# Performance work log

Hardware: AMD Instinct MI355X
Metric: run time of the kernel (lower is better)

Reference implementation:

```python
import jax, jax.numpy as jnp
import numpy as np


def _laplacian(A):
    # D^{-1/2} A D^{-1/2}; original builds diag matrices and does D@A@D,
    # which is mathematically identical to broadcast row/col scaling.
    d = jnp.sum(A, axis=-1)
    dinv = 1.0 / jnp.sqrt(d)
    return A * dinv[:, None] * dinv[None, :]


def _poly(A, theta):
    # P = I + sum_{i=1..k} theta_sig[i-1] * A^i  (theta passed through sigmoid)
    t = jax.nn.sigmoid(theta)
    N = A.shape[-1]
    P = jnp.eye(N, dtype=A.dtype)
    seg = P
    for i in range(theta.shape[0]):  # k is small (2), static loop over poly order
        seg = seg @ A
        P = P + seg * t[i]
    return P


def setup_inputs() -> dict:
    key = jax.random.key(0)
    k1, k2, k3, k4 = jax.random.split(key, 4)
    N, DIN, DOUT, K_CHEB = 4096, 64, 64, 2
    return {
        "x": jax.random.normal(k1, (N, DIN), dtype=jnp.float32),
        "A": jax.random.uniform(k2, (N, N), dtype=jnp.float32),  # positive row sums
        "theta": jax.random.normal(k3, (K_CHEB,), dtype=jnp.float32),
        "W": jax.random.normal(k4, (DOUT, DIN), dtype=jnp.float32) / np.float32(np.sqrt(DIN)),
        "b": jnp.zeros((DOUT,), dtype=jnp.float32),
        "k": 4,
    }


def reference(x, A, theta, W, b, k):
    S = _laplacian(A)
    S = _poly(S, theta)
    S = _laplacian(S)
    # double argsort over last dim = per-row descending rank of each entry
    rank = jnp.argsort(jnp.argsort(-S, axis=-1), axis=-1)
    mask = jnp.where(rank < k, jnp.float32(1.0), jnp.float32(0.0))
    S = S * mask  # keep only top-k entries per row
    x = S @ x     # [N,N] @ [N,DIN]
    return x @ W.T + b  # nn.Linear
```

## Files before the change

### kernel.cpp

```cpp
#include <hip/hip_runtime.h>
#include <hip/hip_bf16.h>
#include <float.h>
#include <math.h>

#define N 4096
#define DIN 64

typedef signed char i8_t;
typedef signed char i8x4 __attribute__((ext_vector_type(4)));
typedef int i32x4 __attribute__((ext_vector_type(4)));
typedef float f32x4 __attribute__((ext_vector_type(4)));

__device__ __forceinline__ void gload16(const void* g, void* l) {
    __builtin_amdgcn_global_load_lds((const __attribute__((address_space(1))) void*)g,
                                     (__attribute__((address_space(3))) void*)l,
                                     16, 0, 0);
}

__device__ __forceinline__ float block_reduce_sum(float s) {
    __shared__ float red[4];
    #pragma unroll
    for (int off = 32; off; off >>= 1) s += __shfl_down(s, off);
    if ((threadIdx.x & 63) == 0) red[threadIdx.x >> 6] = s;
    __syncthreads();
    return red[0] + red[1] + red[2] + red[3];
}

__device__ __forceinline__ bool better(float v1, int j1, float v2, int j2) {
    return v1 > v2 || (v1 == v2 && j1 < j2);
}
__device__ __forceinline__ void ins4(float v, int j, float bv[4], int bj[4]) {
    if (!better(v, j, bv[3], bj[3])) return;
    bv[3] = v; bj[3] = j;
    if (better(bv[3], bj[3], bv[2], bj[2])) {
        float tv = bv[2]; int tj = bj[2]; bv[2] = bv[3]; bj[2] = bj[3]; bv[3] = tv; bj[3] = tj;
    }
    if (better(bv[2], bj[2], bv[1], bj[1])) {
        float tv = bv[1]; int tj = bj[1]; bv[1] = bv[2]; bj[1] = bj[2]; bv[2] = tv; bj[2] = tj;
    }
    if (better(bv[1], bj[1], bv[0], bj[0])) {
        float tv = bv[0]; int tj = bj[0]; bv[0] = bv[1]; bj[0] = bj[1]; bv[1] = tv; bj[1] = tj;
    }
}

__global__ __launch_bounds__(256) void k_rowsum_dinv(const float* __restrict__ A,
                                                     float* __restrict__ dinv,
                                                     float* __restrict__ rowsumP) {
    int row = blockIdx.x, tid = threadIdx.x;
    const float4* a4 = (const float4*)(A + (size_t)row * N);
    float s = 0.f;
    for (int j = tid; j < N / 4; j += 256) {
        float4 v = a4[j];
        s += v.x + v.y + v.z + v.w;
    }
    float tot = block_reduce_sum(s);
    if (tid == 0) {
        dinv[row] = rsqrtf(tot);
        rowsumP[row] = 0.f;
    }
}

__global__ __launch_bounds__(1024) void k_dmax(const float* __restrict__ dinv,
                                               float* __restrict__ dmaxf) {
    int t = threadIdx.x;
    float m = fmaxf(fmaxf(dinv[t], dinv[t + 1024]), fmaxf(dinv[t + 2048], dinv[t + 3072]));
    #pragma unroll
    for (int off = 32; off; off >>= 1) m = fmaxf(m, __shfl_down(m, off));
    __shared__ float red[16];
    if ((t & 63) == 0) red[t >> 6] = m;
    __syncthreads();
    if (t == 0) {
        float mm = red[0];
        #pragma unroll
        for (int i = 1; i < 16; i++) mm = fmaxf(mm, red[i]);
        *dmaxf = mm;
    }
}

__global__ __launch_bounds__(256) void k_make_sqt(const float* __restrict__ A,
                                                  const float* __restrict__ dinv,
                                                  const float* __restrict__ dmaxf,
                                                  i8_t* __restrict__ Sq,
                                                  i8_t* __restrict__ Tq) {
    __shared__ float tile[64][65];
    int tid = threadIdx.x;
    int c4 = tid & 15;
    int rg = tid >> 4;
    int i0 = blockIdx.y * 64;
    int j0 = blockIdx.x * 64;
    float dmax = *dmaxf;
    float sinv = 127.0f / (dmax * dmax);
    float4 dj = *(const float4*)(dinv + j0 + 4 * c4);
    #pragma unroll
    for (int rr = 0; rr < 4; rr++) {
        int r = rg + 16 * rr;
        int row = i0 + r;
        float di = dinv[row];
        float4 av = *(const float4*)(A + (size_t)row * N + j0 + 4 * c4);
        float s0 = av.x * di * dj.x, s1 = av.y * di * dj.y;
        float s2 = av.z * di * dj.z, s3 = av.w * di * dj.w;
        i8x4 qv;
        qv[0] = (i8_t)(int)fminf(rintf(s0 * sinv), 127.f);
        qv[1] = (i8_t)(int)fminf(rintf(s1 * sinv), 127.f);
        qv[2] = (i8_t)(int)fminf(rintf(s2 * sinv), 127.f);
        qv[3] = (i8_t)(int)fminf(rintf(s3 * sinv), 127.f);
        *(i8x4*)(Sq + (size_t)row * N + j0 + 4 * c4) = qv;
        tile[r][4 * c4 + 0] = s0;
        tile[r][4 * c4 + 1] = s1;
        tile[r][4 * c4 + 2] = s2;
        tile[r][4 * c4 + 3] = s3;
    }
    __syncthreads();
    #pragma unroll
    for (int cc = 0; cc < 4; cc++) {
        int c = rg + 16 * cc;
        int gj = j0 + c;
        i8x4 qv;
        #pragma unroll
        for (int u = 0; u < 4; u++)
            qv[u] = (i8_t)(int)fminf(rintf(tile[4 * c4 + u][c] * sinv), 127.f);
        *(i8x4*)(Tq + (size_t)gj * N + i0 + 4 * c4) = qv;
    }
}

__global__ __launch_bounds__(256) void k_gemm(const i8_t* __restrict__ Sq,
                                              const i8_t* __restrict__ Tq,
                                              const float* __restrict__ dmaxf,
                                              const float* __restrict__ theta,
                                              float* __restrict__ rowsumP,
                                              float* __restrict__ candV,
                                              int* __restrict__ candJ) {
    __shared__ i8_t As[128 * 64];
    __shared__ i8_t Bs[128 * 64];
    __shared__ float pbuf[128][65];
    int tid = threadIdx.x;
    int lane = tid & 63;
    int wave = tid >> 6;
    int wr = wave >> 1, wc = wave & 1;
    int bi = blockIdx.x, bj = blockIdx.y;

    int qoff = ((tid & 3) ^ ((tid >> 3) & 3)) * 16;
    int row0 = tid >> 2;
    const i8_t* Ag0 = Sq + (size_t)(bi * 128 + row0) * N + qoff;
    const i8_t* Ag1 = Sq + (size_t)(bi * 128 + 64 + row0) * N + qoff;
    const i8_t* Bg0 = Tq + (size_t)(bj * 128 + row0) * N + qoff;
    const i8_t* Bg1 = Tq + (size_t)(bj * 128 + 64 + row0) * N + qoff;
    i8_t* Al0 = As + tid * 16;
    i8_t* Al1 = As + (tid + 256) * 16;
    i8_t* Bl0 = Bs + tid * 16;
    i8_t* Bl1 = Bs + (tid + 256) * 16;

    i32x4 acc[4][4];
    i32x4 z = {0, 0, 0, 0};
    #pragma unroll
    for (int i = 0; i < 4; i++)
        #pragma unroll
        for (int j = 0; j < 4; j++) acc[i][j] = z;

    int r = lane & 15, q = lane >> 4;
    int qs = q ^ ((r >> 1) & 3);
    int aoff = (wr * 64 + r) * 64 + qs * 16;
    int boff = (wc * 64 + r) * 64 + qs * 16;

    for (int k0 = 0; k0 < N; k0 += 64) {
        __syncthreads();
        gload16(Ag0 + k0, Al0);
        gload16(Ag1 + k0, Al1);
        gload16(Bg0 + k0, Bl0);
        gload16(Bg1 + k0, Bl1);
        __syncthreads();
        i32x4 af[4], bfr[4];
        #pragma unroll
        for (int mi = 0; mi < 4; mi++) af[mi] = *(const i32x4*)(As + aoff + mi * 16 * 64);
        #pragma unroll
        for (int ni = 0; ni < 4; ni++) bfr[ni] = *(const i32x4*)(Bs + boff + ni * 16 * 64);
        #pragma unroll
        for (int mi = 0; mi < 4; mi++)
            #pragma unroll
            for (int ni = 0; ni < 4; ni++)
                acc[mi][ni] = __builtin_amdgcn_mfma_i32_16x16x64_i8(af[mi], bfr[ni],
                                                                    acc[mi][ni], 0, 0, 0);
    }

    float dmax = *dmaxf;
    float sq = dmax * dmax / 127.0f;
    float t0 = 1.f / (1.f + expf(-theta[0]));
    float t1 = 1.f / (1.f + expf(-theta[1]));
    float t0s = t0 * sq;
    float t1s2 = t1 * sq * sq;
    int col = lane & 15, quad = lane >> 4;

    #pragma unroll
    for (int mi = 0; mi < 4; mi++) {
        int gi0 = bi * 128 + wr * 64 + mi * 16 + quad * 4;
        float rsum[4] = {0.f, 0.f, 0.f, 0.f};
        #pragma unroll
        for (int ni = 0; ni < 4; ni++) {
            int gj = bj * 128 + wc * 64 + ni * 16 + col;
            f32x4 pf;
            #pragma unroll
            for (int rr = 0; rr < 4; rr++) {
                int gi = gi0 + rr;
                float qv = (float)Sq[(size_t)gi * N + gj];
                float p = t1s2 * (float)acc[mi][ni][rr] + t0s * qv + ((gi == gj) ? 1.f : 0.f);
                pf[rr] = p;
                rsum[rr] += p;
            }
            acc[mi][ni] = __builtin_bit_cast(i32x4, pf);
        }
        #pragma unroll
        for (int rr = 0; rr < 4; rr++) {
            float v = rsum[rr];
            v += __shfl_xor(v, 1);
            v += __shfl_xor(v, 2);
            v += __shfl_xor(v, 4);
            v += __shfl_xor(v, 8);
            if (col == 0) atomicAdd(&rowsumP[gi0 + rr], v);
        }
    }

    float bv[4] = {-FLT_MAX, -FLT_MAX, -FLT_MAX, -FLT_MAX};
    int bjx[4] = {N, N, N, N};
    int srow = tid >> 1;
    int shalf = tid & 1;

    #pragma unroll
    for (int pass = 0; pass < 2; pass++) {
        if (wc == pass) {
            #pragma unroll
            for (int mi = 0; mi < 4; mi++) {
                int prow = wr * 64 + mi * 16 + quad * 4;
                #pragma unroll
                for (int ni = 0; ni < 4; ni++) {
                    f32x4 pf = __builtin_bit_cast(f32x4, acc[mi][ni]);
                    #pragma unroll
                    for (int rr = 0; rr < 4; rr++)
                        pbuf[prow + rr][ni * 16 + col] = pf[rr];
                }
            }
        }
        __syncthreads();
        int jbase = bj * 128 + pass * 64 + shalf * 32;
        for (int i = 0; i < 32; i++)
            ins4(pbuf[srow][shalf * 32 + i], jbase + i, bv, bjx);
        __syncthreads();
    }

    float ov[4]; int oj[4];
    #pragma unroll
    for (int c = 0; c < 4; c++) { ov[c] = __shfl_xor(bv[c], 1); oj[c] = __shfl_xor(bjx[c], 1); }
    #pragma unroll
    for (int c = 0; c < 4; c++) ins4(ov[c], oj[c], bv, bjx);
    if (shalf == 0) {
        size_t base = ((size_t)(bi * 128 + srow) * 32 + bj) * 4;
        #pragma unroll
        for (int c = 0; c < 4; c++) { candV[base + c] = bv[c]; candJ[base + c] = bjx[c]; }
    }
}

__global__ __launch_bounds__(256) void k_dinv2(const float* __restrict__ rowsumP,
                                               float* __restrict__ dinv2) {
    int g = blockIdx.x * 256 + threadIdx.x;
    dinv2[g] = rsqrtf(rowsumP[g]);
}

__global__ __launch_bounds__(64) void k_final(const float* __restrict__ candV,
                                              const int* __restrict__ candJ,
                                              const float* __restrict__ dinv2,
                                              const float* __restrict__ x,
                                              const float* __restrict__ W,
                                              const float* __restrict__ bvec,
                                              const int* __restrict__ kin,
                                              float* __restrict__ out) {
    int row = blockIdx.x, t = threadIdx.x;
    float2 cv = *(const float2*)(candV + (size_t)row * 128 + t * 2);
    int2 cj = *(const int2*)(candJ + (size_t)row * 128 + t * 2);
    float bv[4] = {-FLT_MAX, -FLT_MAX, -FLT_MAX, -FLT_MAX};
    int bj[4] = {N, N, N, N};
    ins4(cv.x * dinv2[cj.x], cj.x, bv, bj);
    ins4(cv.y * dinv2[cj.y], cj.y, bv, bj);
    #pragma unroll
    for (int off = 1; off < 64; off <<= 1) {
        float ov[4]; int oj[4];
        #pragma unroll
        for (int c = 0; c < 4; c++) { ov[c] = __shfl_xor(bv[c], off); oj[c] = __shfl_xor(bj[c], off); }
        #pragma unroll
        for (int c = 0; c < 4; c++) ins4(ov[c], oj[c], bv, bj);
    }
    int kk = kin[0];
    if (kk > 4) kk = 4;
    if (kk < 0) kk = 0;
    float sc = dinv2[row];
    float y = 0.f;
    for (int c = 0; c < kk; c++)
        y += sc * bv[c] * x[(size_t)bj[c] * DIN + t];
    __shared__ float ys[DIN];
    ys[t] = y;
    __syncthreads();
    const float4* w4 = (const float4*)(W + (size_t)t * DIN);
    const float4* y4 = (const float4*)ys;
    float o = bvec[t];
    #pragma unroll
    for (int d = 0; d < DIN / 4; d++) {
        float4 wv = w4[d], yv = y4[d];
        o += wv.x * yv.x + wv.y * yv.y + wv.z * yv.z + wv.w * yv.w;
    }
    out[(size_t)row * DIN + t] = o;
}

extern "C" void kernel_launch(void* const* d_in, const int* in_sizes, int n_in,
                              void* d_out, int out_size, void* d_ws, size_t ws_size,
                              hipStream_t stream) {
    const float* x = (const float*)d_in[0];
    const float* A = (const float*)d_in[1];
    const float* theta = (const float*)d_in[2];
    const float* W = (const float*)d_in[3];
    const float* b = (const float*)d_in[4];
    const int* kin = (const int*)d_in[5];
    float* out = (float*)d_out;

    char* ws = (char*)d_ws;
    i8_t* Sq = (i8_t*)ws;
    i8_t* Tq = (i8_t*)(ws + (size_t)N * N);
    float* candV = (float*)(ws + (size_t)N * N * 2);
    int* candJ = (int*)(ws + (size_t)N * N * 2 + (size_t)N * 128 * 4);
    float* dinv = (float*)(ws + (size_t)N * N * 2 + (size_t)N * 128 * 8);
    float* dinv2 = dinv + N;
    float* rowsumP = dinv2 + N;
    float* dmaxf = rowsumP + N;

    k_rowsum_dinv<<<N, 256, 0, stream>>>(A, dinv, rowsumP);
    k_dmax<<<1, 1024, 0, stream>>>(dinv, dmaxf);
    k_make_sqt<<<dim3(64, 64), 256, 0, stream>>>(A, dinv, dmaxf, Sq, Tq);
    k_gemm<<<dim3(32, 32), 256, 0, stream>>>(Sq, Tq, dmaxf, theta, rowsumP, candV, candJ);
    k_dinv2<<<N / 256, 256, 0, stream>>>(rowsumP, dinv2);
    k_final<<<N, 64, 0, stream>>>(candV, candJ, dinv2, x, W, b, kin, out);
}
```

Baseline: 277.3 us.

## Double-buffer int8 GEMM LDS tiles by aliasing the epilogue buffer

The int8 MFMA GEMM main loop now uses two LDS stages carved out of the existing pbuf array (128x65 floats, enough for 2x16KB). The next K-tile's global-to-LDS loads are issued before the current tile is consumed, with explicit vmcnt waits and raw s_barrier in place of __syncthreads. Wave priority is raised around the MFMA block. The aim is to overlap global load latency with compute without growing LDS use, at the cost of hand-managed waitcnts that could race if the counts are wrong.

```diff
diff --git a/kernel.cpp b/kernel.cpp
--- a/kernel.cpp
+++ b/kernel.cpp
@@ -130,9 +130,9 @@
                                               float* __restrict__ rowsumP,
                                               float* __restrict__ candV,
                                               int* __restrict__ candJ) {
-    __shared__ i8_t As[128 * 64];
-    __shared__ i8_t Bs[128 * 64];
-    __shared__ float pbuf[128][65];
+    __shared__ __attribute__((aligned(64))) float pbuf[128][65];
+    i8_t* const smem = (i8_t*)pbuf;
+
     int tid = threadIdx.x;
     int lane = tid & 63;
     int wave = tid >> 6;
@@ -145,10 +145,8 @@
     const i8_t* Ag1 = Sq + (size_t)(bi * 128 + 64 + row0) * N + qoff;
     const i8_t* Bg0 = Tq + (size_t)(bj * 128 + row0) * N + qoff;
     const i8_t* Bg1 = Tq + (size_t)(bj * 128 + 64 + row0) * N + qoff;
-    i8_t* Al0 = As + tid * 16;
-    i8_t* Al1 = As + (tid + 256) * 16;
-    i8_t* Bl0 = Bs + tid * 16;
-    i8_t* Bl1 = Bs + (tid + 256) * 16;
+    int l0 = tid * 16;
+    int l1 = (tid + 256) * 16;
 
     i32x4 acc[4][4];
     i32x4 z = {0, 0, 0, 0};
@@ -162,24 +160,46 @@
     int aoff = (wr * 64 + r) * 64 + qs * 16;
     int boff = (wc * 64 + r) * 64 + qs * 16;
 
-    for (int k0 = 0; k0 < N; k0 += 64) {
-        __syncthreads();
-        gload16(Ag0 + k0, Al0);
-        gload16(Ag1 + k0, Al1);
-        gload16(Bg0 + k0, Bl0);
-        gload16(Bg1 + k0, Bl1);
-        __syncthreads();
+    gload16(Ag0, smem + l0);
+    gload16(Ag1, smem + l1);
+    gload16(Bg0, smem + 8192 + l0);
+    gload16(Bg1, smem + 8192 + l1);
+
+    int p = 0;
+    for (int t = 0; t < N / 64; ++t) {
+        int k1 = (t + 1) * 64;
+        if (k1 < N) {
+            i8_t* d = smem + (p ^ 1) * 16384;
+            gload16(Ag0 + k1, d + l0);
+            gload16(Ag1 + k1, d + l1);
+            gload16(Bg0 + k1, d + 8192 + l0);
+            gload16(Bg1 + k1, d + 8192 + l1);
+            asm volatile("s_waitcnt vmcnt(4)" ::: "memory");
+        } else {
+            asm volatile("s_waitcnt vmcnt(0)" ::: "memory");
+        }
+        __builtin_amdgcn_s_barrier();
+
+        const i8_t* Ab = smem + p * 16384;
+        const i8_t* Bb = Ab + 8192;
         i32x4 af[4], bfr[4];
         #pragma unroll
-        for (int mi = 0; mi < 4; mi++) af[mi] = *(const i32x4*)(As + aoff + mi * 16 * 64);
-        #pragma unroll
-        for (int ni = 0; ni < 4; ni++) bfr[ni] = *(const i32x4*)(Bs + boff + ni * 16 * 64);
+        for (int mi = 0; mi < 4; mi++) af[mi] = *(const i32x4*)(Ab + aoff + mi * 16 * 64);
+        #pragma unroll
+        for (int ni = 0; ni < 4; ni++) bfr[ni] = *(const i32x4*)(Bb + boff + ni * 16 * 64);
+
+        __builtin_amdgcn_s_setprio(1);
         #pragma unroll
         for (int mi = 0; mi < 4; mi++)
             #pragma unroll
             for (int ni = 0; ni < 4; ni++)
                 acc[mi][ni] = __builtin_amdgcn_mfma_i32_16x16x64_i8(af[mi], bfr[ni],
                                                                     acc[mi][ni], 0, 0, 0);
+        __builtin_amdgcn_s_setprio(0);
+
+        asm volatile("s_waitcnt lgkmcnt(0)" ::: "memory");
+        __builtin_amdgcn_s_barrier();
+        p ^= 1;
     }
 
     float dmax = *dmaxf;
@@ -202,9 +222,9 @@
             for (int rr = 0; rr < 4; rr++) {
                 int gi = gi0 + rr;
                 float qv = (float)Sq[(size_t)gi * N + gj];
-                float p = t1s2 * (float)acc[mi][ni][rr] + t0s * qv + ((gi == gj) ? 1.f : 0.f);
-                pf[rr] = p;
-                rsum[rr] += p;
+                float p2 = t1s2 * (float)acc[mi][ni][rr] + t0s * qv + ((gi == gj) ? 1.f : 0.f);
+                pf[rr] = p2;
+                rsum[rr] += p2;
             }
             acc[mi][ni] = __builtin_bit_cast(i32x4, pf);
         }
```

Result: faster. 267.3 us (-3.6%).
